# Optimization experiments

Hardware: AMD Instinct MI355X
Metric: run time of the kernel (lower is better)

The kernel has to match this reference:

```python
import jax, jax.numpy as jnp
import numpy as np

TAU = 0.1
B, F_IN, D, K, C = 128, 1000, 512, 10, 5


def setup_inputs() -> dict:
    key = jax.random.key(0)
    ks = jax.random.split(key, 12)
    s = 0.05
    feats = jax.random.normal(ks[0], (B, F_IN), jnp.float32)
    W_adapt = jax.random.normal(ks[1], (F_IN, D), jnp.float32) * s
    b_adapt = jnp.zeros((D,), jnp.float32)
    W_ch = jax.random.normal(ks[2], (C, D, D), jnp.float32) * s   # 5 per-channel Linear(D,D)
    b_ch = jnp.zeros((C, D), jnp.float32)
    W_gate = jax.random.normal(ks[3], (C, D), jnp.float32) * s    # 5 gate Linear(D,1)
    b_gate = jnp.zeros((C,), jnp.float32)
    W_mlp = jax.random.normal(ks[4], (D, K), jnp.float32) * s
    b_mlp = jnp.zeros((K,), jnp.float32)
    T = 1000
    u = jax.random.uniform(ks[5], (B, C, T, 2), jnp.float32, 1e-10, 1.0)
    gumbel = -jnp.log(-jnp.log(u))                                 # Gumbel(0,1) noise, one draw per sample/time
    return {"feats": feats, "W_adapt": W_adapt, "b_adapt": b_adapt,
            "W_ch": W_ch, "b_ch": b_ch, "W_gate": W_gate, "b_gate": b_gate,
            "W_mlp": W_mlp, "b_mlp": b_mlp, "gumbel": gumbel, "repeat_num": T}


def reference(feats, W_adapt, b_adapt, W_ch, b_ch, W_gate, b_gate, W_mlp, b_mlp, gumbel, repeat_num):
    # backbone_output_adapter: Linear(1000, D) + ReLU
    r_b = jax.nn.relu(feats @ W_adapt + b_adapt)                   # [B, D]
    # 5 subjective channels: Linear(D, D) + ReLU each (vectorized over channel axis c)
    h = jax.nn.relu(jnp.einsum('bd,cde->bce', r_b, W_ch) + b_ch)   # [B, C, D]
    # gates: Linear(D, 1) + Sigmoid per channel -> p_t_ [B, C, 1]
    p = jax.nn.sigmoid(jnp.einsum('bcd,cd->bc', h, W_gate) + b_gate)  # [B, C]
    p_t = p[:, :, None]                                            # [B, C, 1]
    # train path: logits = [1-p, p]; repeat_num independent gumbel-softmax draws, vectorized over T
    logits = jnp.stack([1.0 - p, p], axis=-1)                      # [B, C, 2]
    y = jax.nn.softmax((logits[:, :, None, :] + gumbel) / TAU, axis=-1)  # [B, C, T, 2]
    g_t = y[..., 1]                                                # [B, C, T]
    # gate softmax over channel dim, then gated channel mixing
    v_t = jax.nn.softmax(g_t, axis=1)                              # [B, C, T]
    r_g = jnp.einsum('bcd,bct->bdt', h, v_t)                       # [B, D, T]  (256 MB, memory-bound)
    # mlp per time step: Linear(D, K) + ReLU + Softmax(dim=1 over classes)
    logits_s = jax.nn.relu(jnp.einsum('bdt,dk->btk', r_g, W_mlp) + b_mlp)
    r_s = jax.nn.softmax(logits_s, axis=-1)                        # [B, T, K]
    r_s = jnp.transpose(r_s, (1, 0, 2))                            # [T, B, K] == list of T [B,K] outputs
    return (r_s, g_t, p_t)
```

## Files before the change

kernel.cpp:

```cpp
#include <hip/hip_runtime.h>
#include <hip/hip_bf16.h>
#include <math.h>


__global__ __launch_bounds__(256) void kA(const float* __restrict__ feats,
                                          const float* __restrict__ W_adapt,
                                          float* __restrict__ pA) {
    __shared__ float fls[128 * 50];
    __shared__ float wls[50 * 32];
    const int tid = threadIdx.x;
    const int e0 = blockIdx.x * 32;
    const int s  = blockIdx.y;
    const int k0 = s * 50;

    #pragma unroll
    for (int it = 0; it < 25; ++it) {
        int idx = it * 256 + tid;
        int b_l = idx / 50, k_l = idx - b_l * 50;
        fls[idx] = feats[b_l * 1000 + k0 + k_l];
    }
    #pragma unroll
    for (int it = 0; it < 7; ++it) {
        int idx = it * 256 + tid;
        if (idx < 1600)
            wls[idx] = W_adapt[(k0 + (idx >> 5)) * 512 + e0 + (idx & 31)];
    }
    __syncthreads();

    const int ep = tid & 15, bg = tid >> 4;
    float2 acc[8] = {};
    const float* fb = &fls[bg * 8 * 50];
    const float* wb = &wls[ep * 2];
    #pragma unroll 2
    for (int k = 0; k < 50; ++k) {
        float2 w = *(const float2*)&wb[k * 32];
        #pragma unroll
        for (int i = 0; i < 8; ++i) {
            float r = fb[i * 50 + k];
            acc[i].x = fmaf(r, w.x, acc[i].x);
            acc[i].y = fmaf(r, w.y, acc[i].y);
        }
    }
    #pragma unroll
    for (int i = 0; i < 8; ++i)
        *(float2*)&pA[(s * 128 + bg * 8 + i) * 512 + e0 + ep * 2] = acc[i];
}

__global__ __launch_bounds__(256) void kRA(const float* __restrict__ pA,
                                           const float* __restrict__ b_adapt,
                                           float* __restrict__ r_b) {
    int i = blockIdx.x * 256 + threadIdx.x;
    float acc = b_adapt[i & 511];
    #pragma unroll
    for (int s = 0; s < 20; ++s) acc += pA[s * 65536 + i];
    r_b[i] = fmaxf(acc, 0.f);
}

__global__ __launch_bounds__(256) void kB(const float* __restrict__ r_b,
                                          const float* __restrict__ W_ch,
                                          float* __restrict__ pB) {
    __shared__ float rbs[128 * 64];
    __shared__ float wls[64 * 32];
    const int tid = threadIdx.x;
    const int e0 = blockIdx.x * 32;
    const int ds = blockIdx.y;
    const int c  = blockIdx.z;
    const int d0 = ds * 64;

    #pragma unroll
    for (int it = 0; it < 32; ++it) {
        int idx = it * 256 + tid;
        rbs[idx] = r_b[(idx >> 6) * 512 + d0 + (idx & 63)];
    }
    #pragma unroll
    for (int it = 0; it < 8; ++it) {
        int idx = it * 256 + tid;
        wls[idx] = W_ch[((size_t)(c * 512 + d0 + (idx >> 5))) * 512 + e0 + (idx & 31)];
    }
    __syncthreads();

    const int ep = tid & 15, bg = tid >> 4;
    float2 acc[8] = {};
    const float* rb = &rbs[bg * 8 * 64];
    const float* wb = &wls[ep * 2];
    #pragma unroll 2
    for (int d = 0; d < 64; ++d) {
        float2 w = *(const float2*)&wb[d * 32];
        #pragma unroll
        for (int i = 0; i < 8; ++i) {
            float r = rb[i * 64 + d];
            acc[i].x = fmaf(r, w.x, acc[i].x);
            acc[i].y = fmaf(r, w.y, acc[i].y);
        }
    }
    #pragma unroll
    for (int i = 0; i < 8; ++i)
        *(float2*)&pB[((ds * 5 + c) * 128 + bg * 8 + i) * 512 + e0 + ep * 2] = acc[i];
}

__global__ __launch_bounds__(512) void kCG(const float* __restrict__ pB,
                                           const float* __restrict__ b_ch,
                                           const float* __restrict__ W_gate,
                                           const float* __restrict__ W_mlp,
                                           const float* __restrict__ b_gate,
                                           const float* __restrict__ b_mlp,
                                           const float* __restrict__ gumbel,
                                           float* __restrict__ out_rs,
                                           float* __restrict__ out_gt,
                                           float* __restrict__ out_pt) {
    __shared__ float sWm[5120];
    __shared__ float red[5][11];
    __shared__ float spv[5], sM[50];
    const int tid = threadIdx.x;
    const int tc = blockIdx.x, b = blockIdx.y;

    #pragma unroll
    for (int it = 0; it < 10; ++it) sWm[it * 512 + tid] = W_mlp[it * 512 + tid];
    __syncthreads();

    const int wv = tid >> 6, lane = tid & 63;
    if (wv < 5) {
        const int c = wv;
        float gs = 0.f, am[10] = {};
        #pragma unroll
        for (int i = 0; i < 8; ++i) {
            int e = i * 64 + lane;
            float hs = b_ch[c * 512 + e];
            #pragma unroll
            for (int s = 0; s < 8; ++s)
                hs += pB[((s * 5 + c) * 128 + b) * 512 + e];
            float h = fmaxf(hs, 0.f);
            gs = fmaf(h, W_gate[c * 512 + e], gs);
            const float* wm = &sWm[e * 10];
            #pragma unroll
            for (int k = 0; k < 10; ++k) am[k] = fmaf(h, wm[k], am[k]);
        }
        #pragma unroll
        for (int off = 32; off; off >>= 1) {
            gs += __shfl_xor(gs, off);
            #pragma unroll
            for (int k = 0; k < 10; ++k) am[k] += __shfl_xor(am[k], off);
        }
        if (lane == 0) {
            red[c][0] = gs;
            #pragma unroll
            for (int k = 0; k < 10; ++k) red[c][1 + k] = am[k];
        }
    }
    __syncthreads();
    if (tid < 5) {
        float pv = 1.f / (1.f + __expf(-(red[tid][0] + b_gate[tid])));
        spv[tid] = pv;
        if (tc == 0) out_pt[b * 5 + tid] = pv;
    }
    if (tid < 50) sM[tid] = red[tid / 10][1 + tid % 10];
    __syncthreads();

    int t = tc * 500 + tid;
    if (tid >= 500) return;
    float ex[5], ssum = 0.f;
    #pragma unroll
    for (int c = 0; c < 5; ++c) {
        float2 gu = *(const float2*)&gumbel[(size_t)(((b * 5 + c) * 1000) + t) * 2];
        float arg = (2.f * spv[c] - 1.f + gu.y - gu.x) * 10.0f;
        float gt  = 1.f / (1.f + __expf(-arg));
        out_gt[(b * 5 + c) * 1000 + t] = gt;
        float e = __expf(gt);
        ex[c] = e; ssum += e;
    }
    float inv = 1.f / ssum;
    float lg[10];
    #pragma unroll
    for (int k = 0; k < 10; ++k) lg[k] = b_mlp[k];
    #pragma unroll
    for (int c = 0; c < 5; ++c) {
        float v = ex[c] * inv;
        #pragma unroll
        for (int k = 0; k < 10; ++k) lg[k] = fmaf(v, sM[c * 10 + k], lg[k]);
    }
    float mx = 0.f;
    #pragma unroll
    for (int k = 0; k < 10; ++k) { lg[k] = fmaxf(lg[k], 0.f); mx = fmaxf(mx, lg[k]); }
    float se = 0.f;
    #pragma unroll
    for (int k = 0; k < 10; ++k) { lg[k] = __expf(lg[k] - mx); se += lg[k]; }
    float invs = 1.f / se;
    float2 outv[5];
    #pragma unroll
    for (int k = 0; k < 10; ++k) ((float*)outv)[k] = lg[k] * invs;
    float2* dst = (float2*)&out_rs[(size_t)t * 1280 + b * 10];
    #pragma unroll
    for (int j = 0; j < 5; ++j) dst[j] = outv[j];
}

extern "C" void kernel_launch(void* const* d_in, const int* in_sizes, int n_in,
                              void* d_out, int out_size, void* d_ws, size_t ws_size,
                              hipStream_t stream) {
    const float* feats   = (const float*)d_in[0];
    const float* W_adapt = (const float*)d_in[1];
    const float* b_adapt = (const float*)d_in[2];
    const float* W_ch    = (const float*)d_in[3];
    const float* b_ch    = (const float*)d_in[4];
    const float* W_gate  = (const float*)d_in[5];
    const float* b_gate  = (const float*)d_in[6];
    const float* W_mlp   = (const float*)d_in[7];
    const float* b_mlp   = (const float*)d_in[8];
    const float* gumbel  = (const float*)d_in[9];

    float* out    = (float*)d_out;
    float* out_rs = out;
    float* out_gt = out + 1280000;
    float* out_pt = out + 1920000;

    float* ws  = (float*)d_ws;
    float* pA  = ws;
    float* pB  = pA + 1310720;
    float* r_b = pB + 2621440;

    kA <<<dim3(16, 20),   256, 0, stream>>>(feats, W_adapt, pA);
    kRA<<<256,            256, 0, stream>>>(pA, b_adapt, r_b);
    kB <<<dim3(16, 8, 5), 256, 0, stream>>>(r_b, W_ch, pB);
    kCG<<<dim3(2, 128),   512, 0, stream>>>(pB, b_ch, W_gate, W_mlp, b_gate,
                                            b_mlp, gumbel, out_rs, out_gt, out_pt);
}
```

Baseline: 42.12 us.

## Widen kB output tile with transposed r_b in LDS; merge kCG time chunks per batch

kB now computes a 64-wide output tile per block, with each thread producing float4 outputs. r_b is stored transposed in LDS with padding so the inner loop reads contiguous rows, and the grid is halved. kCG processes both halves of the time axis in one block per batch row, so the channel/gate reduction over pB is no longer done twice. This removes redundant loads and compute, but it also halves the number of blocks in both kernels, leaving fewer resident blocks to hide latency on a large GPU.

```diff
diff --git a/kernel.cpp b/kernel.cpp
--- a/kernel.cpp
+++ b/kernel.cpp
@@ -59,10 +59,10 @@
 __global__ __launch_bounds__(256) void kB(const float* __restrict__ r_b,
                                           const float* __restrict__ W_ch,
                                           float* __restrict__ pB) {
-    __shared__ float rbs[128 * 64];
-    __shared__ float wls[64 * 32];
+    __shared__ float rbs[64 * 129];
+    __shared__ float wls[64 * 64];
     const int tid = threadIdx.x;
-    const int e0 = blockIdx.x * 32;
+    const int e0 = blockIdx.x * 64;
     const int ds = blockIdx.y;
     const int c  = blockIdx.z;
     const int d0 = ds * 64;
@@ -70,32 +70,34 @@
     #pragma unroll
     for (int it = 0; it < 32; ++it) {
         int idx = it * 256 + tid;
-        rbs[idx] = r_b[(idx >> 6) * 512 + d0 + (idx & 63)];
-    }
-    #pragma unroll
-    for (int it = 0; it < 8; ++it) {
-        int idx = it * 256 + tid;
-        wls[idx] = W_ch[((size_t)(c * 512 + d0 + (idx >> 5))) * 512 + e0 + (idx & 31)];
+        int b = idx >> 6, d = idx & 63;
+        rbs[d * 129 + b] = r_b[b * 512 + d0 + d];
+    }
+    #pragma unroll
+    for (int it = 0; it < 16; ++it) {
+        int idx = it * 256 + tid;
+        wls[idx] = W_ch[((size_t)(c * 512 + d0 + (idx >> 6))) * 512 + e0 + (idx & 63)];
     }
     __syncthreads();
 
     const int ep = tid & 15, bg = tid >> 4;
-    float2 acc[8] = {};
-    const float* rb = &rbs[bg * 8 * 64];
-    const float* wb = &wls[ep * 2];
+    float4 acc[8] = {};
     #pragma unroll 2
     for (int d = 0; d < 64; ++d) {
-        float2 w = *(const float2*)&wb[d * 32];
+        float4 w = *(const float4*)&wls[d * 64 + ep * 4];
+        const float* rr = &rbs[d * 129 + bg * 8];
         #pragma unroll
         for (int i = 0; i < 8; ++i) {
-            float r = rb[i * 64 + d];
+            float r = rr[i];
             acc[i].x = fmaf(r, w.x, acc[i].x);
             acc[i].y = fmaf(r, w.y, acc[i].y);
+            acc[i].z = fmaf(r, w.z, acc[i].z);
+            acc[i].w = fmaf(r, w.w, acc[i].w);
         }
     }
     #pragma unroll
     for (int i = 0; i < 8; ++i)
-        *(float2*)&pB[((ds * 5 + c) * 128 + bg * 8 + i) * 512 + e0 + ep * 2] = acc[i];
+        *(float4*)&pB[((ds * 5 + c) * 128 + bg * 8 + i) * 512 + e0 + ep * 4] = acc[i];
 }
 
 __global__ __launch_bounds__(512) void kCG(const float* __restrict__ pB,
@@ -112,7 +114,7 @@
     __shared__ float red[5][11];
     __shared__ float spv[5], sM[50];
     const int tid = threadIdx.x;
-    const int tc = blockIdx.x, b = blockIdx.y;
+    const int b = blockIdx.x;
 
     #pragma unroll
     for (int it = 0; it < 10; ++it) sWm[it * 512 + tid] = W_mlp[it * 512 + tid];
@@ -151,46 +153,50 @@
     if (tid < 5) {
         float pv = 1.f / (1.f + __expf(-(red[tid][0] + b_gate[tid])));
         spv[tid] = pv;
-        if (tc == 0) out_pt[b * 5 + tid] = pv;
+        out_pt[b * 5 + tid] = pv;
     }
     if (tid < 50) sM[tid] = red[tid / 10][1 + tid % 10];
     __syncthreads();
 
-    int t = tc * 500 + tid;
-    if (tid >= 500) return;
-    float ex[5], ssum = 0.f;
-    #pragma unroll
-    for (int c = 0; c < 5; ++c) {
-        float2 gu = *(const float2*)&gumbel[(size_t)(((b * 5 + c) * 1000) + t) * 2];
-        float arg = (2.f * spv[c] - 1.f + gu.y - gu.x) * 10.0f;
-        float gt  = 1.f / (1.f + __expf(-arg));
-        out_gt[(b * 5 + c) * 1000 + t] = gt;
-        float e = __expf(gt);
-        ex[c] = e; ssum += e;
-    }
-    float inv = 1.f / ssum;
-    float lg[10];
-    #pragma unroll
-    for (int k = 0; k < 10; ++k) lg[k] = b_mlp[k];
-    #pragma unroll
-    for (int c = 0; c < 5; ++c) {
-        float v = ex[c] * inv;
-        #pragma unroll
-        for (int k = 0; k < 10; ++k) lg[k] = fmaf(v, sM[c * 10 + k], lg[k]);
-    }
-    float mx = 0.f;
-    #pragma unroll
-    for (int k = 0; k < 10; ++k) { lg[k] = fmaxf(lg[k], 0.f); mx = fmaxf(mx, lg[k]); }
-    float se = 0.f;
-    #pragma unroll
-    for (int k = 0; k < 10; ++k) { lg[k] = __expf(lg[k] - mx); se += lg[k]; }
-    float invs = 1.f / se;
-    float2 outv[5];
-    #pragma unroll
-    for (int k = 0; k < 10; ++k) ((float*)outv)[k] = lg[k] * invs;
-    float2* dst = (float2*)&out_rs[(size_t)t * 1280 + b * 10];
-    #pragma unroll
-    for (int j = 0; j < 5; ++j) dst[j] = outv[j];
+    #pragma unroll
+    for (int rep = 0; rep < 2; ++rep) {
+        if (tid < 500) {
+            int t = rep * 500 + tid;
+            float ex[5], ssum = 0.f;
+            #pragma unroll
+            for (int c = 0; c < 5; ++c) {
+                float2 gu = *(const float2*)&gumbel[(size_t)(((b * 5 + c) * 1000) + t) * 2];
+                float arg = (2.f * spv[c] - 1.f + gu.y - gu.x) * 10.0f;
+                float gt  = 1.f / (1.f + __expf(-arg));
+                out_gt[(b * 5 + c) * 1000 + t] = gt;
+                float e = __expf(gt);
+                ex[c] = e; ssum += e;
+            }
+            float inv = 1.f / ssum;
+            float lg[10];
+            #pragma unroll
+            for (int k = 0; k < 10; ++k) lg[k] = b_mlp[k];
+            #pragma unroll
+            for (int c = 0; c < 5; ++c) {
+                float v = ex[c] * inv;
+                #pragma unroll
+                for (int k = 0; k < 10; ++k) lg[k] = fmaf(v, sM[c * 10 + k], lg[k]);
+            }
+            float mx = 0.f;
+            #pragma unroll
+            for (int k = 0; k < 10; ++k) { lg[k] = fmaxf(lg[k], 0.f); mx = fmaxf(mx, lg[k]); }
+            float se = 0.f;
+            #pragma unroll
+            for (int k = 0; k < 10; ++k) { lg[k] = __expf(lg[k] - mx); se += lg[k]; }
+            float invs = 1.f / se;
+            float2 outv[5];
+            #pragma unroll
+            for (int k = 0; k < 10; ++k) ((float*)outv)[k] = lg[k] * invs;
+            float2* dst = (float2*)&out_rs[(size_t)t * 1280 + b * 10];
+            #pragma unroll
+            for (int j = 0; j < 5; ++j) dst[j] = outv[j];
+        }
+    }
 }
 
 extern "C" void kernel_launch(void* const* d_in, const int* in_sizes, int n_in,
@@ -217,9 +223,9 @@
     float* pB  = pA + 1310720;
     float* r_b = pB + 2621440;
 
-    kA <<<dim3(16, 20),   256, 0, stream>>>(feats, W_adapt, pA);
-    kRA<<<256,            256, 0, stream>>>(pA, b_adapt, r_b);
-    kB <<<dim3(16, 8, 5), 256, 0, stream>>>(r_b, W_ch, pB);
-    kCG<<<dim3(2, 128),   512, 0, stream>>>(pB, b_ch, W_gate, W_mlp, b_gate,
-                                            b_mlp, gumbel, out_rs, out_gt, out_pt);
-}
+    kA <<<dim3(16, 20),  256, 0, stream>>>(feats, W_adapt, pA);
+    kRA<<<256,           256, 0, stream>>>(pA, b_adapt, r_b);
+    kB <<<dim3(8, 8, 5), 256, 0, stream>>>(r_b, W_ch, pB);
+    kCG<<<128,           512, 0, stream>>>(pB, b_ch, W_gate, W_mlp, b_gate,
+                                           b_mlp, gumbel, out_rs, out_gt, out_pt);
+}
```

Measured after the change: 43.68 us. +3.7%, slower.
